# Performance work log

Measured on AMD Instinct MI355X. Metric: run time of the kernel, lower is better.

Reference implementation:

```python
import jax, jax.numpy as jnp
import numpy as np
from jax import lax

B, T, D_IN, D_H, D_OUT = 64, 512, 256, 1024, 256


def setup_inputs() -> dict:
    key = jax.random.key(0)
    k1, k2, k3, k4 = jax.random.split(key, 4)
    # lecun_normal-style scaling: std = 1/sqrt(fan_in)
    inputs = jax.random.normal(k1, (B, T, D_IN), dtype=jnp.float32)
    input_kernel = jax.random.normal(k2, (D_IN, D_H), dtype=jnp.float32) / np.sqrt(D_IN)
    hidden_kernel = jax.random.normal(k3, (D_H, D_H), dtype=jnp.float32) / np.sqrt(D_H)
    hidden_bias = jnp.zeros((D_H,), dtype=jnp.float32)
    output_kernel = jax.random.normal(k4, (D_H, D_OUT), dtype=jnp.float32) / np.sqrt(D_H)
    output_bias = jnp.zeros((D_OUT,), dtype=jnp.float32)
    return {
        "inputs": inputs,
        "input_kernel": input_kernel,
        "hidden_kernel": hidden_kernel,
        "hidden_bias": hidden_bias,
        "output_kernel": output_kernel,
        "output_bias": output_bias,
    }


def reference(inputs, input_kernel, hidden_kernel, hidden_bias, output_kernel, output_bias):
    # inputs: [B, T, D_in]. Precompute the input projection for all timesteps
    # (batched GEMM) — same math as per-step x_t @ W_in inside scan.
    x_proj = jnp.einsum("bti,ih->bth", inputs, input_kernel) + hidden_bias  # [B,T,H]
    x_proj_tm = jnp.swapaxes(x_proj, 0, 1)  # time-major [T,B,H]

    def step(h, xp_t):
        h_new = jnp.tanh(xp_t + jnp.dot(h, hidden_kernel))  # [B,H]
        return h_new, h_new

    h0 = jnp.zeros((inputs.shape[0], hidden_kernel.shape[0]), dtype=inputs.dtype)
    _, hidden_states = lax.scan(step, h0, x_proj_tm)  # [T,B,H]
    hidden_states = jnp.swapaxes(hidden_states, 0, 1)  # [B,T,H]
    # Dense readout applied to every timestep (return_sequences=True)
    outputs = jnp.einsum("bth,ho->bto", hidden_states, output_kernel) + output_bias
    return outputs
```

## Files before the change

kernel.cpp:

```cpp
#include <hip/hip_runtime.h>
#include <stdint.h>
#include <stddef.h>


#define TT 512
#define HH 1024

typedef __attribute__((ext_vector_type(8))) short short8;
typedef __attribute__((ext_vector_type(4))) float f32x4;
typedef unsigned long long u64;

#define POISON 0xAAAAAAAAAAAAAAAAull

__device__ __forceinline__ short f2bf(float f) {
  uint32_t u = __builtin_bit_cast(uint32_t, f);
  u += 0x7fffu + ((u >> 16) & 1u);
  return (short)(u >> 16);
}

__device__ __forceinline__ float fast_tanh(float x) {
  float ax = fabsf(x);
  float e = __expf(-2.f * ax);
  float r = (1.f - e) * __builtin_amdgcn_rcpf(1.f + e);
  return copysignf(r, x);
}

__device__ __forceinline__ u64 ald(const u64* p) {
  return __hip_atomic_load(p, __ATOMIC_RELAXED, __HIP_MEMORY_SCOPE_AGENT);
}
__device__ __forceinline__ void ast(u64* p, u64 v) {
  __hip_atomic_store(p, v, __ATOMIC_RELAXED, __HIP_MEMORY_SCOPE_AGENT);
}

__global__ __launch_bounds__(256, 2) void rnn_fused(
    const float* __restrict__ inp, const float* __restrict__ w_in,
    const float* __restrict__ w_h, const float* __restrict__ h_b,
    const float* __restrict__ w_o, const float* __restrict__ o_b,
    float* __restrict__ xp, short* __restrict__ hbuf,
    float* __restrict__ out) {
  __shared__ __attribute__((aligned(16))) char smem[18688];
  const int blk = blockIdx.x;
  const int tid = threadIdx.x;
  const int wv = tid >> 6, l = tid & 63, lr = l & 15, lq = l >> 4;

  if (blk < 64) {
    const int g = blk & 3, j = blk >> 2;
    const int ntg = j * 4 + wv;

    f32x4 (*red)[4][64] = (f32x4 (*)[4][64])smem;
    short (*tr)[72] = (short (*)[72])(smem + 16384);

    short8 wf[8][4];
#pragma unroll
    for (int f = 0; f < 8; ++f)
#pragma unroll
      for (int nt = 0; nt < 4; ++nt) {
        int n = j * 64 + nt * 16 + lr;
        int k0 = wv * 256 + f * 32 + lq * 8;
        short8 v;
#pragma unroll
        for (int e = 0; e < 8; ++e) v[e] = f2bf(w_h[(size_t)(k0 + e) * HH + n]);
        wf[f][nt] = v;
      }

    const u64* hq = (const u64*)hbuf;
    u64* hqw = (u64*)hbuf;
    const u64* xq = (const u64*)xp;

    for (int t = 0; t < TT; ++t) {
      size_t xb = ((size_t)(t * 4 + g) * 64 + ntg) * 128 + (size_t)l * 2;
      u64 x0 = ald(xq + xb), x1 = ald(xq + xb + 1);

      f32x4 acc[4];
#pragma unroll
      for (int nt = 0; nt < 4; ++nt) acc[nt] = (f32x4){0.f, 0.f, 0.f, 0.f};

      if (t > 0) {
        u64 q[16];
        size_t base = (((size_t)((t - 1) * 4 + g) * 32 + wv * 8) * 64 + l) * 2;
        int bad;
        do {
#pragma unroll
          for (int f = 0; f < 8; ++f) {
            q[2 * f]     = ald(hq + base + (size_t)f * 128);
            q[2 * f + 1] = ald(hq + base + (size_t)f * 128 + 1);
          }
          int mybad = 0;
#pragma unroll
          for (int i = 0; i < 16; ++i) mybad |= (q[i] == POISON);
          bad = __any(mybad);
        } while (bad);

        short8 af[8];
#pragma unroll
        for (int f = 0; f < 8; ++f) {
          union { u64 qq[2]; short8 s; } u;
          u.qq[0] = q[2 * f];
          u.qq[1] = q[2 * f + 1];
          af[f] = u.s;
        }
#pragma unroll
        for (int f = 0; f < 8; ++f)
#pragma unroll
          for (int nt = 0; nt < 4; ++nt)
            acc[nt] = __builtin_amdgcn_mfma_f32_16x16x32_bf16(af[f], wf[f][nt], acc[nt], 0, 0, 0);
      }

      red[wv][0][l] = acc[0];
      red[wv][1][l] = acc[1];
      red[wv][2][l] = acc[2];
      red[wv][3][l] = acc[3];
      __syncthreads();
      f32x4 tot = red[0][wv][l] + red[1][wv][l] + red[2][wv][l] + red[3][wv][l];

      while (__any((x0 == POISON) | (x1 == POISON))) {
        x0 = ald(xq + xb);
        x1 = ald(xq + xb + 1);
      }
      union { u64 qq[2]; f32x4 v; } xu;
      xu.qq[0] = x0;
      xu.qq[1] = x1;

#pragma unroll
      for (int i2 = 0; i2 < 4; ++i2) {
        float v = tot[i2] + xu.v[i2];
        tr[lq * 4 + i2][wv * 16 + lr] = f2bf(fast_tanh(v));
      }
      __syncthreads();

      if (wv < 2) {
        short8 hv = *(const short8*)&tr[lr][wv * 32 + lq * 8];
        union { short8 s; u64 qq[2]; } u;
        u.s = hv;
        size_t wbase = (((size_t)(t * 4 + g) * 32 + (j * 2 + wv)) * 64 + l) * 2;
        ast(hqw + wbase, u.qq[0]);
        ast(hqw + wbase + 1, u.qq[1]);
      }
    }
  } else {
    const int w = blk - 64;
    const int c = w & 3, s48 = w >> 2;

    {
      short* ldsA = (short*)smem;

      short8 wfx[8][4];
#pragma unroll
      for (int kt = 0; kt < 8; ++kt)
#pragma unroll
        for (int nt = 0; nt < 4; ++nt) {
          int col = c * 256 + (wv * 4 + nt) * 16 + lr;
          int k0 = kt * 32 + lq * 8;
          short8 v;
#pragma unroll
          for (int e = 0; e < 8; ++e) v[e] = f2bf(w_in[(size_t)(k0 + e) * HH + col]);
          wfx[kt][nt] = v;
        }
      float bias[4];
#pragma unroll
      for (int nt = 0; nt < 4; ++nt) bias[nt] = h_b[c * 256 + (wv * 4 + nt) * 16 + lr];

      u64* xqw = (u64*)xp;
      for (int k = 0; k < 43; ++k) {
        int m = s48 + 48 * k;
        if (m >= 2048) break;
        int t = m >> 2, g2 = m & 3;
        {
          int row = tid >> 4, cb = (tid & 15) * 16;
          const float* src = inp + ((size_t)(g2 * 16 + row) * TT + t) * 256 + cb;
          f32x4 v0 = *(const f32x4*)(src);
          f32x4 v1 = *(const f32x4*)(src + 4);
          f32x4 v2 = *(const f32x4*)(src + 8);
          f32x4 v3 = *(const f32x4*)(src + 12);
          short8 sa, sb;
          sa[0]=f2bf(v0[0]); sa[1]=f2bf(v0[1]); sa[2]=f2bf(v0[2]); sa[3]=f2bf(v0[3]);
          sa[4]=f2bf(v1[0]); sa[5]=f2bf(v1[1]); sa[6]=f2bf(v1[2]); sa[7]=f2bf(v1[3]);
          sb[0]=f2bf(v2[0]); sb[1]=f2bf(v2[1]); sb[2]=f2bf(v2[2]); sb[3]=f2bf(v2[3]);
          sb[4]=f2bf(v3[0]); sb[5]=f2bf(v3[1]); sb[6]=f2bf(v3[2]); sb[7]=f2bf(v3[3]);
          *(short8*)&ldsA[row * 264 + cb] = sa;
          *(short8*)&ldsA[row * 264 + cb + 8] = sb;
        }
        __syncthreads();

        f32x4 acc[4];
#pragma unroll
        for (int nt = 0; nt < 4; ++nt) acc[nt] = (f32x4){0.f, 0.f, 0.f, 0.f};
#pragma unroll
        for (int kt = 0; kt < 8; ++kt) {
          short8 a = *(const short8*)&ldsA[lr * 264 + kt * 32 + lq * 8];
#pragma unroll
          for (int nt = 0; nt < 4; ++nt)
            acc[nt] = __builtin_amdgcn_mfma_f32_16x16x32_bf16(a, wfx[kt][nt], acc[nt], 0, 0, 0);
        }
#pragma unroll
        for (int nt = 0; nt < 4; ++nt) {
          union { f32x4 v; u64 qq[2]; } u;
#pragma unroll
          for (int i2 = 0; i2 < 4; ++i2) u.v[i2] = acc[nt][i2] + bias[nt];
          size_t base =
              ((size_t)(t * 4 + g2) * 64 + c * 16 + wv * 4 + nt) * 128 + (size_t)l * 2;
          ast(xqw + base, u.qq[0]);
          ast(xqw + base + 1, u.qq[1]);
        }
        __syncthreads();
      }
    }

    {
      f32x4 (*red)[4][64] = (f32x4 (*)[4][64])smem;

      short8 wfo[8][4];
#pragma unroll
      for (int f = 0; f < 8; ++f)
#pragma unroll
        for (int nt = 0; nt < 4; ++nt) {
          int o = c * 64 + nt * 16 + lr;
          int k0 = wv * 256 + f * 32 + lq * 8;
          short8 v;
#pragma unroll
          for (int e = 0; e < 8; ++e) v[e] = f2bf(w_o[(size_t)(k0 + e) * 256 + o]);
          wfo[f][nt] = v;
        }
      float bias = o_b[c * 64 + wv * 16 + lr];
      const u64* hq = (const u64*)hbuf;

      for (int k = 0; k < 43; ++k) {
        int m = s48 + 48 * k;
        if (m >= 2048) break;
        int t = m >> 2, g2 = m & 3;

        u64 q[16];
        size_t base = (((size_t)(t * 4 + g2) * 32 + wv * 8) * 64 + l) * 2;
        for (;;) {
          q[0] = ald(hq + base);
          q[1] = ald(hq + base + 1);
          if (!__any((q[0] == POISON) | (q[1] == POISON))) break;
          __builtin_amdgcn_s_sleep(32);
        }
        int bad;
        do {
#pragma unroll
          for (int f = 1; f < 8; ++f) {
            q[2 * f]     = ald(hq + base + (size_t)f * 128);
            q[2 * f + 1] = ald(hq + base + (size_t)f * 128 + 1);
          }
          int mybad = 0;
#pragma unroll
          for (int i = 2; i < 16; ++i) mybad |= (q[i] == POISON);
          bad = __any(mybad);
          if (bad) __builtin_amdgcn_s_sleep(8);
        } while (bad);

        short8 af[8];
#pragma unroll
        for (int f = 0; f < 8; ++f) {
          union { u64 qq[2]; short8 s; } u;
          u.qq[0] = q[2 * f];
          u.qq[1] = q[2 * f + 1];
          af[f] = u.s;
        }
        f32x4 acc[4];
#pragma unroll
        for (int nt = 0; nt < 4; ++nt) acc[nt] = (f32x4){0.f, 0.f, 0.f, 0.f};
#pragma unroll
        for (int f = 0; f < 8; ++f)
#pragma unroll
          for (int nt = 0; nt < 4; ++nt)
            acc[nt] = __builtin_amdgcn_mfma_f32_16x16x32_bf16(af[f], wfo[f][nt], acc[nt], 0, 0, 0);

        red[wv][0][l] = acc[0];
        red[wv][1][l] = acc[1];
        red[wv][2][l] = acc[2];
        red[wv][3][l] = acc[3];
        __syncthreads();
        f32x4 tot = red[0][wv][l] + red[1][wv][l] + red[2][wv][l] + red[3][wv][l];
#pragma unroll
        for (int i2 = 0; i2 < 4; ++i2) {
          int b = g2 * 16 + lq * 4 + i2;
          out[((size_t)b * TT + t) * 256 + c * 64 + wv * 16 + lr] = tot[i2] + bias;
        }
        __syncthreads();
      }
    }
  }
}

extern "C" void kernel_launch(void* const* d_in, const int* in_sizes, int n_in,
                              void* d_out, int out_size, void* d_ws, size_t ws_size,
                              hipStream_t stream) {
  const float* inp  = (const float*)d_in[0];
  const float* w_in = (const float*)d_in[1];
  const float* w_h  = (const float*)d_in[2];
  const float* h_b  = (const float*)d_in[3];
  const float* w_o  = (const float*)d_in[4];
  const float* o_b  = (const float*)d_in[5];

  float* xp   = (float*)d_ws;
  short* hbuf = (short*)((char*)d_ws + (size_t)134217728);

  rnn_fused<<<256, 256, 0, stream>>>(inp, w_in, w_h, h_b, w_o, o_b, xp, hbuf,
                                     (float*)d_out);
}
```

Baseline: 1.248 ms.

## Split recurrent GEMV over full K per wave to drop LDS reduction and barriers

Each wave of the recurrent blocks now owns 16 output columns across the whole K=1024 dimension, holding 32 bf16 weight fragments in registers. This removes the cross-wave LDS reduction and both __syncthreads per timestep. The cost is that every wave must load the full previous hidden state. The x-projection for the next timestep is prefetched one step ahead, and the grid shrinks to 192 blocks with launch_bounds occupancy 1, leaving 128 worker blocks instead of 192. Register pressure goes up (32 weight fragments plus 64 u64 loads) and the input and output phases get fewer workers.

```diff
diff --git a/kernel.cpp b/kernel.cpp
--- a/kernel.cpp
+++ b/kernel.cpp
@@ -32,13 +32,13 @@
   __hip_atomic_store(p, v, __ATOMIC_RELAXED, __HIP_MEMORY_SCOPE_AGENT);
 }
 
-__global__ __launch_bounds__(256, 2) void rnn_fused(
+__global__ __launch_bounds__(256, 1) void rnn_fused(
     const float* __restrict__ inp, const float* __restrict__ w_in,
     const float* __restrict__ w_h, const float* __restrict__ h_b,
     const float* __restrict__ w_o, const float* __restrict__ o_b,
     float* __restrict__ xp, short* __restrict__ hbuf,
     float* __restrict__ out) {
-  __shared__ __attribute__((aligned(16))) char smem[18688];
+  __shared__ __attribute__((aligned(16))) char smem[16384];
   const int blk = blockIdx.x;
   const int tid = threadIdx.x;
   const int wv = tid >> 6, l = tid & 63, lr = l & 15, lq = l >> 4;
@@ -47,71 +47,59 @@
     const int g = blk & 3, j = blk >> 2;
     const int ntg = j * 4 + wv;
 
-    f32x4 (*red)[4][64] = (f32x4 (*)[4][64])smem;
-    short (*tr)[72] = (short (*)[72])(smem + 16384);
-
-    short8 wf[8][4];
-#pragma unroll
-    for (int f = 0; f < 8; ++f)
-#pragma unroll
-      for (int nt = 0; nt < 4; ++nt) {
-        int n = j * 64 + nt * 16 + lr;
-        int k0 = wv * 256 + f * 32 + lq * 8;
-        short8 v;
-#pragma unroll
-        for (int e = 0; e < 8; ++e) v[e] = f2bf(w_h[(size_t)(k0 + e) * HH + n]);
-        wf[f][nt] = v;
-      }
+    short (*tile)[16][24] = (short (*)[16][24])smem;
+
+    short8 wf[32];
+#pragma unroll
+    for (int f = 0; f < 32; ++f) {
+      int n = j * 64 + wv * 16 + lr;
+      int k0 = f * 32 + lq * 8;
+      short8 v;
+#pragma unroll
+      for (int e = 0; e < 8; ++e) v[e] = f2bf(w_h[(size_t)(k0 + e) * HH + n]);
+      wf[f] = v;
+    }
 
     const u64* hq = (const u64*)hbuf;
     u64* hqw = (u64*)hbuf;
     const u64* xq = (const u64*)xp;
 
+    const int f0 = j * 2 + (wv >> 1);
+    const int ltgt = ((wv & 1) * 2 + (l >> 4)) * 16 + (l & 15);
+
+    size_t xb = ((size_t)g * 64 + ntg) * 128 + (size_t)l * 2;
+    u64 x0 = ald(xq + xb), x1 = ald(xq + xb + 1);
+
     for (int t = 0; t < TT; ++t) {
-      size_t xb = ((size_t)(t * 4 + g) * 64 + ntg) * 128 + (size_t)l * 2;
-      u64 x0 = ald(xq + xb), x1 = ald(xq + xb + 1);
-
       f32x4 acc[4];
 #pragma unroll
-      for (int nt = 0; nt < 4; ++nt) acc[nt] = (f32x4){0.f, 0.f, 0.f, 0.f};
+      for (int i = 0; i < 4; ++i) acc[i] = (f32x4){0.f, 0.f, 0.f, 0.f};
 
       if (t > 0) {
-        u64 q[16];
-        size_t base = (((size_t)((t - 1) * 4 + g) * 32 + wv * 8) * 64 + l) * 2;
+        const size_t sb = ((size_t)((t - 1) * 4 + g) * 2048 + l) * 2;
+        u64 q[64];
         int bad;
         do {
 #pragma unroll
-          for (int f = 0; f < 8; ++f) {
-            q[2 * f]     = ald(hq + base + (size_t)f * 128);
-            q[2 * f + 1] = ald(hq + base + (size_t)f * 128 + 1);
+          for (int f = 0; f < 32; ++f) {
+            q[2 * f]     = ald(hq + sb + (size_t)f * 128);
+            q[2 * f + 1] = ald(hq + sb + (size_t)f * 128 + 1);
           }
           int mybad = 0;
 #pragma unroll
-          for (int i = 0; i < 16; ++i) mybad |= (q[i] == POISON);
+          for (int i = 0; i < 64; ++i) mybad |= (q[i] == POISON);
           bad = __any(mybad);
         } while (bad);
 
-        short8 af[8];
-#pragma unroll
-        for (int f = 0; f < 8; ++f) {
+#pragma unroll
+        for (int f = 0; f < 32; ++f) {
           union { u64 qq[2]; short8 s; } u;
           u.qq[0] = q[2 * f];
           u.qq[1] = q[2 * f + 1];
-          af[f] = u.s;
-        }
-#pragma unroll
-        for (int f = 0; f < 8; ++f)
-#pragma unroll
-          for (int nt = 0; nt < 4; ++nt)
-            acc[nt] = __builtin_amdgcn_mfma_f32_16x16x32_bf16(af[f], wf[f][nt], acc[nt], 0, 0, 0);
-      }
-
-      red[wv][0][l] = acc[0];
-      red[wv][1][l] = acc[1];
-      red[wv][2][l] = acc[2];
-      red[wv][3][l] = acc[3];
-      __syncthreads();
-      f32x4 tot = red[0][wv][l] + red[1][wv][l] + red[2][wv][l] + red[3][wv][l];
+          acc[f & 3] = __builtin_amdgcn_mfma_f32_16x16x32_bf16(u.s, wf[f], acc[f & 3], 0, 0, 0);
+        }
+      }
+      f32x4 tot = (acc[0] + acc[1]) + (acc[2] + acc[3]);
 
       while (__any((x0 == POISON) | (x1 == POISON))) {
         x0 = ald(xq + xb);
@@ -120,26 +108,30 @@
       union { u64 qq[2]; f32x4 v; } xu;
       xu.qq[0] = x0;
       xu.qq[1] = x1;
+      if (t + 1 < TT) {
+        xb = ((size_t)((t + 1) * 4 + g) * 64 + ntg) * 128 + (size_t)l * 2;
+        x0 = ald(xq + xb);
+        x1 = ald(xq + xb + 1);
+      }
 
 #pragma unroll
       for (int i2 = 0; i2 < 4; ++i2) {
         float v = tot[i2] + xu.v[i2];
-        tr[lq * 4 + i2][wv * 16 + lr] = f2bf(fast_tanh(v));
-      }
-      __syncthreads();
-
-      if (wv < 2) {
-        short8 hv = *(const short8*)&tr[lr][wv * 32 + lq * 8];
+        tile[wv][lq * 4 + i2][lr] = f2bf(fast_tanh(v));
+      }
+
+      if (l < 32) {
+        short8 hv = *(const short8*)&tile[wv][l & 15][(l >> 4) * 8];
         union { short8 s; u64 qq[2]; } u;
         u.s = hv;
-        size_t wbase = (((size_t)(t * 4 + g) * 32 + (j * 2 + wv)) * 64 + l) * 2;
+        size_t wbase = (((size_t)(t * 4 + g) * 32 + f0) * 64 + ltgt) * 2;
         ast(hqw + wbase, u.qq[0]);
         ast(hqw + wbase + 1, u.qq[1]);
       }
     }
   } else {
     const int w = blk - 64;
-    const int c = w & 3, s48 = w >> 2;
+    const int c = w & 3, s = w >> 2;
 
     {
       short* ldsA = (short*)smem;
@@ -161,9 +153,8 @@
       for (int nt = 0; nt < 4; ++nt) bias[nt] = h_b[c * 256 + (wv * 4 + nt) * 16 + lr];
 
       u64* xqw = (u64*)xp;
-      for (int k = 0; k < 43; ++k) {
-        int m = s48 + 48 * k;
-        if (m >= 2048) break;
+      for (int k = 0; k < 64; ++k) {
+        int m = s + 32 * k;
         int t = m >> 2, g2 = m & 3;
         {
           int row = tid >> 4, cb = (tid & 15) * 16;
@@ -224,9 +215,8 @@
       float bias = o_b[c * 64 + wv * 16 + lr];
       const u64* hq = (const u64*)hbuf;
 
-      for (int k = 0; k < 43; ++k) {
-        int m = s48 + 48 * k;
-        if (m >= 2048) break;
+      for (int k = 0; k < 64; ++k) {
+        int m = s + 32 * k;
         int t = m >> 2, g2 = m & 3;
 
         u64 q[16];
@@ -298,6 +288,6 @@
   float* xp   = (float*)d_ws;
   short* hbuf = (short*)((char*)d_ws + (size_t)134217728);
 
-  rnn_fused<<<256, 256, 0, stream>>>(inp, w_in, w_h, h_b, w_o, o_b, xp, hbuf,
+  rnn_fused<<<192, 256, 0, stream>>>(inp, w_in, w_h, h_b, w_o, o_b, xp, hbuf,
                                      (float*)d_out);
 }
```

Measured after the change: 2.973 ms. +138.3%, slower.
